# Performance work log

Hardware: AMD Instinct MI355X
Metric: run time of the kernel (lower is better)

Reference implementation:

```python
import jax, jax.numpy as jnp
import numpy as np

VOCAB = 50000
D = 256       # text_latent_size
E = 20000     # num_of_evidences
L = 20        # words_in_question / words per evidence sentence


def position_encoding(L, D):
    # encoding[i, j] = 1 - i/L - (j/D) * (1 - 2*i/L)
    i = jnp.arange(L, dtype=jnp.float32)[:, None] / L
    j = jnp.arange(D, dtype=jnp.float32)[None, :] / D
    return 1.0 - i - j * (1.0 - 2.0 * i)  # [L, D]


def setup_inputs() -> dict:
    key = jax.random.key(0)
    ks = jax.random.split(key, 8)
    evidence = jax.random.randint(ks[0], (E, L), 0, VOCAB)
    question = jax.random.randint(ks[1], (1, L), 0, VOCAB)
    scale = 0.05
    q_table = jax.random.normal(ks[2], (VOCAB, D), dtype=jnp.float32) * scale
    e_table = jax.random.normal(ks[3], (VOCAB, D), dtype=jnp.float32) * scale
    te1 = jax.random.normal(ks[4], (E, D), dtype=jnp.float32) * scale
    te2 = jax.random.normal(ks[5], (E, D), dtype=jnp.float32) * scale
    W = jax.random.normal(ks[6], (VOCAB, D), dtype=jnp.float32) * scale
    b = jax.random.normal(ks[7], (VOCAB,), dtype=jnp.float32) * scale
    return {"evidence": evidence, "question": question, "q_table": q_table,
            "e_table": e_table, "te1": te1, "te2": te2, "W": W, "b": b}


def reference(evidence, question, q_table, e_table, te1, te2, W, b):
    pe = position_encoding(L, D)                            # [L, D]
    # question: embed, position-encode, sum over words -> [D]
    q_emb = (q_table[question[0]] * pe).sum(axis=0)         # [D]
    # evidence: two embeddings, position-encode, sum over words -> [E, D]
    ev_comp = (q_table[evidence] * pe[None]).sum(axis=1) + te2  # [E, D]
    ev_feat = (e_table[evidence] * pe[None]).sum(axis=1) + te1  # [E, D]
    # attention over memories
    scores = ev_comp @ q_emb                                 # [E]
    weights = jax.nn.softmax(scores)                         # [E]
    weighted = weights @ ev_feat                             # [D]
    features = weighted + q_emb                              # [D]
    logits = features @ W.T + b                              # [VOCAB]
    return jax.nn.softmax(logits)
```

## Files before the change

### kernel.cpp

```cpp
#include <hip/hip_runtime.h>

#define D      256
#define L_W    20
#define E_CNT  20000
#define VOCAB  50000

#define CHUNK   1024
#define NCHUNK  49
#define NSLICE  8
#define RPS     (E_CNT / NSLICE)
#define PSTRIDE (NCHUNK * CHUNK)
#define WTB     256

#define OFF_QEMB  0
#define OFF_X     256
#define OFF_Y     512
#define OFF_WTE1  768
#define OFF_SUMW  1024
#define OFF_SUML  1025
#define OFF_A     1032
#define OFF_B     (OFF_A + VOCAB)
#define OFF_P     (OFF_B + VOCAB)
#define OFF_Q     (OFF_P + VOCAB)
#define OFF_EXPW  (OFF_Q + VOCAB)
#define OFF_EXPL  (OFF_EXPW + E_CNT)
#define OFF_PPART (OFF_EXPL + VOCAB)
#define OFF_QPART (OFF_PPART + NSLICE * PSTRIDE)
#define OFF_WTP   (OFF_QPART + NSLICE * PSTRIDE)
#define WS_FLOATS (OFF_WTP + WTB * D)

__device__ __forceinline__ float wave_reduce(float v) {
#pragma unroll
    for (int o = 32; o > 0; o >>= 1) v += __shfl_xor(v, o, 64);
    return v;
}

__device__ __forceinline__ float u_of(int j) { return 1.f - (float)j * (1.f / 128.f); }
__device__ __forceinline__ float s_of(int j) { return (float)j * (1.f / 256.f); }

__global__ void k1_qemb(const int* __restrict__ question,
                        const float* __restrict__ q_table,
                        float* __restrict__ ws) {
    __shared__ int sQ[L_W];
    int tid = threadIdx.x;
    if (tid < L_W) sQ[tid] = question[tid];
    __syncthreads();
    int j = tid;
    float u = u_of(j), s = s_of(j);
    float acc = 0.f;
#pragma unroll
    for (int i = 0; i < L_W; ++i) {
        float a = 1.f - (float)i * (1.f / (float)L_W);
        acc += q_table[(size_t)sQ[i] * D + j] * (a * u + s);
    }
    ws[OFF_QEMB + j] = acc;
    ws[OFF_X + j] = 0.f;
    ws[OFF_Y + j] = 0.f;
    ws[OFF_WTE1 + j] = 0.f;
    if (tid == 0) { ws[OFF_SUMW] = 0.f; ws[OFF_SUML] = 0.f; }
}

__global__ void k2_ab(const float* __restrict__ q_table, float* __restrict__ ws) {
    __shared__ float sQE[D];
    int tid = threadIdx.x;
    sQE[tid] = ws[OFF_QEMB + tid];
    __syncthreads();
    int wv = tid >> 6, lane = tid & 63;
    int v = blockIdx.x * 4 + wv;
    int j0 = lane * 4;
    const float4 q = *reinterpret_cast<const float4*>(&q_table[(size_t)v * D + j0]);
    float qe0 = sQE[j0], qe1 = sQE[j0 + 1], qe2 = sQE[j0 + 2], qe3 = sQE[j0 + 3];
    float accA = q.x * (u_of(j0) * qe0) + q.y * (u_of(j0 + 1) * qe1) +
                 q.z * (u_of(j0 + 2) * qe2) + q.w * (u_of(j0 + 3) * qe3);
    float accB = q.x * (s_of(j0) * qe0) + q.y * (s_of(j0 + 1) * qe1) +
                 q.z * (s_of(j0 + 2) * qe2) + q.w * (s_of(j0 + 3) * qe3);
    accA = wave_reduce(accA);
    accB = wave_reduce(accB);
    if (lane == 0) {
        ws[OFF_A + v] = accA;
        ws[OFF_B + v] = accB;
        ws[OFF_P + v] = 0.f;
        ws[OFF_Q + v] = 0.f;
    }
}

__global__ void k3_scores(const int* __restrict__ evidence,
                          const float* __restrict__ te2,
                          float* __restrict__ ws) {
    __shared__ float sQE[D];
    __shared__ float sPart[4];
    int tid = threadIdx.x;
    sQE[tid] = ws[OFF_QEMB + tid];
    __syncthreads();
    int wv = tid >> 6, lane = tid & 63;
    int gw = blockIdx.x * 4 + wv;
    int stride = gridDim.x * 4;
    int j0 = lane * 4;
    const float4 qe = *reinterpret_cast<const float4*>(&sQE[j0]);
    float wsum = 0.f;
    for (int e = gw; e < E_CNT; e += stride) {
        const float4 t = *reinterpret_cast<const float4*>(&te2[(size_t)e * D + j0]);
        float p = t.x * qe.x + t.y * qe.y + t.z * qe.z + t.w * qe.w;
        if (lane < 2 * L_W) {
            int l = (lane < L_W) ? lane : (lane - L_W);
            int idx = evidence[e * L_W + l];
            if (lane < L_W) {
                float a = 1.f - (float)l * (1.f / (float)L_W);
                p += a * ws[OFF_A + idx];
            } else {
                p += ws[OFF_B + idx];
            }
        }
        float s_e = wave_reduce(p);
        float ex = expf(s_e);
        if (lane == 0) ws[OFF_EXPW + e] = ex;
        wsum += ex;
    }
    if (lane == 0) sPart[wv] = wsum;
    __syncthreads();
    if (tid == 0) atomicAdd(&ws[OFF_SUMW], sPart[0] + sPart[1] + sPart[2] + sPart[3]);
}

__global__ void k5_scatter2(const int* __restrict__ evidence, float* __restrict__ ws) {
    __shared__ float sP[CHUNK], sQ[CHUNK];
    int tid = threadIdx.x;
    int chunk = blockIdx.x % NCHUNK;
    int slice = blockIdx.x / NCHUNK;
    for (int i = tid; i < CHUNK; i += 256) { sP[i] = 0.f; sQ[i] = 0.f; }
    __syncthreads();
    int lo = chunk * CHUNK;
    float inv = 1.f / ws[OFF_SUMW];
    int r0 = slice * RPS;
    for (int r = tid; r < RPS; r += 256) {
        int e = r0 + r;
        float w = ws[OFF_EXPW + e] * inv;
        const int4* rp = reinterpret_cast<const int4*>(evidence + (size_t)e * L_W);
        int4 v0 = rp[0], v1 = rp[1], v2 = rp[2], v3 = rp[3], v4 = rp[4];
        int idxs[L_W] = {v0.x, v0.y, v0.z, v0.w, v1.x, v1.y, v1.z, v1.w,
                         v2.x, v2.y, v2.z, v2.w, v3.x, v3.y, v3.z, v3.w,
                         v4.x, v4.y, v4.z, v4.w};
#pragma unroll
        for (int l = 0; l < L_W; ++l) {
            int d = idxs[l] - lo;
            if ((unsigned)d < (unsigned)CHUNK) {
                float a = 1.f - (float)l * (1.f / (float)L_W);
                atomicAdd(&sP[d], w * a);
                atomicAdd(&sQ[d], w);
            }
        }
    }
    __syncthreads();
    float* pp = &ws[OFF_PPART + (size_t)slice * PSTRIDE + (size_t)chunk * CHUNK];
    float* qp = &ws[OFF_QPART + (size_t)slice * PSTRIDE + (size_t)chunk * CHUNK];
    for (int i = tid; i < CHUNK; i += 256) { pp[i] = sP[i]; qp[i] = sQ[i]; }
}

__global__ void k5c_wte1(const float* __restrict__ te1, float* __restrict__ ws) {
    __shared__ float sWT[D];
    int tid = threadIdx.x;
    sWT[tid] = 0.f;
    __syncthreads();
    float inv = 1.f / ws[OFF_SUMW];
    int wv = tid >> 6, lane = tid & 63;
    int gw = blockIdx.x * 4 + wv;
    int stride = gridDim.x * 4;
    int j0 = lane * 4;
    float a0 = 0.f, a1 = 0.f, a2 = 0.f, a3 = 0.f;
    for (int e = gw; e < E_CNT; e += stride) {
        float w = ws[OFF_EXPW + e] * inv;
        const float4 t = *reinterpret_cast<const float4*>(&te1[(size_t)e * D + j0]);
        a0 += w * t.x; a1 += w * t.y; a2 += w * t.z; a3 += w * t.w;
    }
    atomicAdd(&sWT[j0 + 0], a0);
    atomicAdd(&sWT[j0 + 1], a1);
    atomicAdd(&sWT[j0 + 2], a2);
    atomicAdd(&sWT[j0 + 3], a3);
    __syncthreads();
    ws[OFF_WTP + blockIdx.x * D + tid] = sWT[tid];
}

__global__ void k5b_reduce(float* __restrict__ ws) {
    int tid = threadIdx.x;
    int v = blockIdx.x * 256 + tid;
    if (v < VOCAB) {
        float p = 0.f, q = 0.f;
#pragma unroll
        for (int s = 0; s < NSLICE; ++s) {
            p += ws[OFF_PPART + s * PSTRIDE + v];
            q += ws[OFF_QPART + s * PSTRIDE + v];
        }
        ws[OFF_P + v] = p;
        ws[OFF_Q + v] = q;
    }
    if (blockIdx.x == 0) {
        float acc = 0.f;
        for (int b = 0; b < WTB; ++b) acc += ws[OFF_WTP + b * D + tid];
        ws[OFF_WTE1 + tid] = acc;
    }
}

__global__ void k5_scatter(const int* __restrict__ evidence,
                           const float* __restrict__ te1,
                           float* __restrict__ ws) {
    __shared__ float sWT[D];
    int tid = threadIdx.x;
    sWT[tid] = 0.f;
    __syncthreads();
    float inv = 1.f / ws[OFF_SUMW];
    int wv = tid >> 6, lane = tid & 63;
    int gw = blockIdx.x * 4 + wv;
    int stride = gridDim.x * 4;
    int j0 = lane * 4;
    float a0 = 0.f, a1 = 0.f, a2 = 0.f, a3 = 0.f;
    for (int e = gw; e < E_CNT; e += stride) {
        float w = ws[OFF_EXPW + e] * inv;
        const float4 t = *reinterpret_cast<const float4*>(&te1[(size_t)e * D + j0]);
        a0 += w * t.x; a1 += w * t.y; a2 += w * t.z; a3 += w * t.w;
        if (lane < L_W) {
            int idx = evidence[e * L_W + lane];
            float a = 1.f - (float)lane * (1.f / (float)L_W);
            atomicAdd(&ws[OFF_P + idx], w * a);
            atomicAdd(&ws[OFF_Q + idx], w);
        }
    }
    atomicAdd(&sWT[j0 + 0], a0);
    atomicAdd(&sWT[j0 + 1], a1);
    atomicAdd(&sWT[j0 + 2], a2);
    atomicAdd(&sWT[j0 + 3], a3);
    __syncthreads();
    atomicAdd(&ws[OFF_WTE1 + tid], sWT[tid]);
}

__global__ void k6_xy(const float* __restrict__ e_table, float* __restrict__ ws) {
    __shared__ float sX[D], sY[D];
    int tid = threadIdx.x;
    sX[tid] = 0.f;
    sY[tid] = 0.f;
    __syncthreads();
    int wv = tid >> 6, lane = tid & 63;
    int gw = blockIdx.x * 4 + wv;
    int stride = gridDim.x * 4;
    int j0 = lane * 4;
    float x0 = 0.f, x1 = 0.f, x2 = 0.f, x3 = 0.f;
    float y0 = 0.f, y1 = 0.f, y2 = 0.f, y3 = 0.f;
    for (int v = gw; v < VOCAB; v += stride) {
        float P = ws[OFF_P + v];
        float Q = ws[OFF_Q + v];
        const float4 t = *reinterpret_cast<const float4*>(&e_table[(size_t)v * D + j0]);
        x0 += P * t.x; x1 += P * t.y; x2 += P * t.z; x3 += P * t.w;
        y0 += Q * t.x; y1 += Q * t.y; y2 += Q * t.z; y3 += Q * t.w;
    }
    atomicAdd(&sX[j0 + 0], x0); atomicAdd(&sX[j0 + 1], x1);
    atomicAdd(&sX[j0 + 2], x2); atomicAdd(&sX[j0 + 3], x3);
    atomicAdd(&sY[j0 + 0], y0); atomicAdd(&sY[j0 + 1], y1);
    atomicAdd(&sY[j0 + 2], y2); atomicAdd(&sY[j0 + 3], y3);
    __syncthreads();
    atomicAdd(&ws[OFF_X + tid], sX[tid]);
    atomicAdd(&ws[OFF_Y + tid], sY[tid]);
}

__global__ void k8_logits(const float* __restrict__ Wm, const float* __restrict__ bv,
                          float* __restrict__ ws) {
    __shared__ float sF[D];
    __shared__ float sPart[4];
    int tid = threadIdx.x;
    {
        int j = tid;
        sF[j] = u_of(j) * ws[OFF_X + j] + s_of(j) * ws[OFF_Y + j] +
                ws[OFF_WTE1 + j] + ws[OFF_QEMB + j];
    }
    __syncthreads();
    int wv = tid >> 6, lane = tid & 63;
    int gw = blockIdx.x * 4 + wv;
    int stride = gridDim.x * 4;
    int j0 = lane * 4;
    const float4 f = *reinterpret_cast<const float4*>(&sF[j0]);
    float lsum = 0.f;
    for (int v = gw; v < VOCAB; v += stride) {
        const float4 w4 = *reinterpret_cast<const float4*>(&Wm[(size_t)v * D + j0]);
        float p = w4.x * f.x + w4.y * f.y + w4.z * f.z + w4.w * f.w;
        float logit = wave_reduce(p) + bv[v];
        float ex = expf(logit);
        if (lane == 0) ws[OFF_EXPL + v] = ex;
        lsum += ex;
    }
    if (lane == 0) sPart[wv] = lsum;
    __syncthreads();
    if (tid == 0) atomicAdd(&ws[OFF_SUML], sPart[0] + sPart[1] + sPart[2] + sPart[3]);
}

__global__ void k10_norm(float* __restrict__ out, const float* __restrict__ ws) {
    int i = blockIdx.x * 256 + threadIdx.x;
    if (i < VOCAB) out[i] = ws[OFF_EXPL + i] * (1.f / ws[OFF_SUML]);
}

extern "C" void kernel_launch(void* const* d_in, const int* in_sizes, int n_in,
                              void* d_out, int out_size, void* d_ws, size_t ws_size,
                              hipStream_t stream) {
    const int*   evidence = (const int*)d_in[0];
    const int*   question = (const int*)d_in[1];
    const float* q_table  = (const float*)d_in[2];
    const float* e_table  = (const float*)d_in[3];
    const float* te1      = (const float*)d_in[4];
    const float* te2      = (const float*)d_in[5];
    const float* Wm       = (const float*)d_in[6];
    const float* bv       = (const float*)d_in[7];
    float* out = (float*)d_out;
    float* ws  = (float*)d_ws;

    const bool big = ws_size >= (size_t)WS_FLOATS * sizeof(float);

    k1_qemb<<<1, 256, 0, stream>>>(question, q_table, ws);
    k2_ab<<<VOCAB / 4, 256, 0, stream>>>(q_table, ws);
    k3_scores<<<512, 256, 0, stream>>>(evidence, te2, ws);
    if (big) {
        k5_scatter2<<<NCHUNK * NSLICE, 256, 0, stream>>>(evidence, ws);
        k5c_wte1<<<WTB, 256, 0, stream>>>(te1, ws);
        k5b_reduce<<<(VOCAB + 255) / 256, 256, 0, stream>>>(ws);
    } else {
        k5_scatter<<<512, 256, 0, stream>>>(evidence, te1, ws);
    }
    k6_xy<<<1024, 256, 0, stream>>>(e_table, ws);
    k8_logits<<<1024, 256, 0, stream>>>(Wm, bv, ws);
    k10_norm<<<(VOCAB + 255) / 256, 256, 0, stream>>>(out, ws);
}
```

Before: 296.0 us.

## Fuse te1 weighting into e_table pass and replace global atomics with partial reductions

The separate te1-weighted-sum kernel is removed and its work folded into the e_table X/Y accumulation kernel, which now walks a combined row range and processes four rows per iteration. Global float atomics for the softmax denominators and the X/Y accumulators become per-block partial buffers, reduced by a new reduction kernel or inside the consuming kernels. Softmax normalisation of the evidence weights is deferred to the logits kernel, and the scatter slice count is halved. This trades a kernel launch and atomic contention for an extra small reduction kernel and redundant per-block reductions in the logits and normalisation kernels.

```diff
diff --git a/kernel.cpp b/kernel.cpp
--- a/kernel.cpp
+++ b/kernel.cpp
@@ -4,21 +4,24 @@
 #define L_W    20
 #define E_CNT  20000
 #define VOCAB  50000
+#define TOTROW (VOCAB + E_CNT)
 
 #define CHUNK   1024
 #define NCHUNK  49
-#define NSLICE  8
+#define NSLICE  4
 #define RPS     (E_CNT / NSLICE)
 #define PSTRIDE (NCHUNK * CHUNK)
-#define WTB     256
+
+#define K6_BLOCKS 512
+#define K6_STRIDE 768
 
 #define OFF_QEMB  0
 #define OFF_X     256
 #define OFF_Y     512
 #define OFF_WTE1  768
-#define OFF_SUMW  1024
-#define OFF_SUML  1025
-#define OFF_A     1032
+#define OFF_SWP   1024
+#define OFF_LP    1536
+#define OFF_A     2560
 #define OFF_B     (OFF_A + VOCAB)
 #define OFF_P     (OFF_B + VOCAB)
 #define OFF_Q     (OFF_P + VOCAB)
@@ -26,8 +29,8 @@
 #define OFF_EXPL  (OFF_EXPW + E_CNT)
 #define OFF_PPART (OFF_EXPL + VOCAB)
 #define OFF_QPART (OFF_PPART + NSLICE * PSTRIDE)
-#define OFF_WTP   (OFF_QPART + NSLICE * PSTRIDE)
-#define WS_FLOATS (OFF_WTP + WTB * D)
+#define OFF_XYP   (OFF_QPART + NSLICE * PSTRIDE)
+#define WS_FLOATS (OFF_XYP + K6_BLOCKS * K6_STRIDE)
 
 __device__ __forceinline__ float wave_reduce(float v) {
 #pragma unroll
@@ -54,10 +57,6 @@
         acc += q_table[(size_t)sQ[i] * D + j] * (a * u + s);
     }
     ws[OFF_QEMB + j] = acc;
-    ws[OFF_X + j] = 0.f;
-    ws[OFF_Y + j] = 0.f;
-    ws[OFF_WTE1 + j] = 0.f;
-    if (tid == 0) { ws[OFF_SUMW] = 0.f; ws[OFF_SUML] = 0.f; }
 }
 
 __global__ void k2_ab(const float* __restrict__ q_table, float* __restrict__ ws) {
@@ -118,7 +117,7 @@
     }
     if (lane == 0) sPart[wv] = wsum;
     __syncthreads();
-    if (tid == 0) atomicAdd(&ws[OFF_SUMW], sPart[0] + sPart[1] + sPart[2] + sPart[3]);
+    if (tid == 0) ws[OFF_SWP + blockIdx.x] = sPart[0] + sPart[1] + sPart[2] + sPart[3];
 }
 
 __global__ void k5_scatter2(const int* __restrict__ evidence, float* __restrict__ ws) {
@@ -129,11 +128,10 @@
     for (int i = tid; i < CHUNK; i += 256) { sP[i] = 0.f; sQ[i] = 0.f; }
     __syncthreads();
     int lo = chunk * CHUNK;
-    float inv = 1.f / ws[OFF_SUMW];
     int r0 = slice * RPS;
     for (int r = tid; r < RPS; r += 256) {
         int e = r0 + r;
-        float w = ws[OFF_EXPW + e] * inv;
+        float w = ws[OFF_EXPW + e];
         const int4* rp = reinterpret_cast<const int4*>(evidence + (size_t)e * L_W);
         int4 v0 = rp[0], v1 = rp[1], v2 = rp[2], v3 = rp[3], v4 = rp[4];
         int idxs[L_W] = {v0.x, v0.y, v0.z, v0.w, v1.x, v1.y, v1.z, v1.w,
@@ -155,33 +153,8 @@
     for (int i = tid; i < CHUNK; i += 256) { pp[i] = sP[i]; qp[i] = sQ[i]; }
 }
 
-__global__ void k5c_wte1(const float* __restrict__ te1, float* __restrict__ ws) {
-    __shared__ float sWT[D];
-    int tid = threadIdx.x;
-    sWT[tid] = 0.f;
-    __syncthreads();
-    float inv = 1.f / ws[OFF_SUMW];
-    int wv = tid >> 6, lane = tid & 63;
-    int gw = blockIdx.x * 4 + wv;
-    int stride = gridDim.x * 4;
-    int j0 = lane * 4;
-    float a0 = 0.f, a1 = 0.f, a2 = 0.f, a3 = 0.f;
-    for (int e = gw; e < E_CNT; e += stride) {
-        float w = ws[OFF_EXPW + e] * inv;
-        const float4 t = *reinterpret_cast<const float4*>(&te1[(size_t)e * D + j0]);
-        a0 += w * t.x; a1 += w * t.y; a2 += w * t.z; a3 += w * t.w;
-    }
-    atomicAdd(&sWT[j0 + 0], a0);
-    atomicAdd(&sWT[j0 + 1], a1);
-    atomicAdd(&sWT[j0 + 2], a2);
-    atomicAdd(&sWT[j0 + 3], a3);
-    __syncthreads();
-    ws[OFF_WTP + blockIdx.x * D + tid] = sWT[tid];
-}
-
 __global__ void k5b_reduce(float* __restrict__ ws) {
-    int tid = threadIdx.x;
-    int v = blockIdx.x * 256 + tid;
+    int v = blockIdx.x * 256 + threadIdx.x;
     if (v < VOCAB) {
         float p = 0.f, q = 0.f;
 #pragma unroll
@@ -192,30 +165,15 @@
         ws[OFF_P + v] = p;
         ws[OFF_Q + v] = q;
     }
-    if (blockIdx.x == 0) {
-        float acc = 0.f;
-        for (int b = 0; b < WTB; ++b) acc += ws[OFF_WTP + b * D + tid];
-        ws[OFF_WTE1 + tid] = acc;
-    }
-}
-
-__global__ void k5_scatter(const int* __restrict__ evidence,
-                           const float* __restrict__ te1,
-                           float* __restrict__ ws) {
-    __shared__ float sWT[D];
-    int tid = threadIdx.x;
-    sWT[tid] = 0.f;
-    __syncthreads();
-    float inv = 1.f / ws[OFF_SUMW];
+}
+
+__global__ void k5_scatter(const int* __restrict__ evidence, float* __restrict__ ws) {
+    int tid = threadIdx.x;
     int wv = tid >> 6, lane = tid & 63;
     int gw = blockIdx.x * 4 + wv;
     int stride = gridDim.x * 4;
-    int j0 = lane * 4;
-    float a0 = 0.f, a1 = 0.f, a2 = 0.f, a3 = 0.f;
     for (int e = gw; e < E_CNT; e += stride) {
-        float w = ws[OFF_EXPW + e] * inv;
-        const float4 t = *reinterpret_cast<const float4*>(&te1[(size_t)e * D + j0]);
-        a0 += w * t.x; a1 += w * t.y; a2 += w * t.z; a3 += w * t.w;
+        float w = ws[OFF_EXPW + e];
         if (lane < L_W) {
             int idx = evidence[e * L_W + lane];
             float a = 1.f - (float)lane * (1.f / (float)L_W);
@@ -223,52 +181,109 @@
             atomicAdd(&ws[OFF_Q + idx], w);
         }
     }
-    atomicAdd(&sWT[j0 + 0], a0);
-    atomicAdd(&sWT[j0 + 1], a1);
-    atomicAdd(&sWT[j0 + 2], a2);
-    atomicAdd(&sWT[j0 + 3], a3);
-    __syncthreads();
-    atomicAdd(&ws[OFF_WTE1 + tid], sWT[tid]);
-}
-
-__global__ void k6_xy(const float* __restrict__ e_table, float* __restrict__ ws) {
-    __shared__ float sX[D], sY[D];
-    int tid = threadIdx.x;
-    sX[tid] = 0.f;
-    sY[tid] = 0.f;
+}
+
+__global__ void k6_xyt(const float* __restrict__ e_table,
+                       const float* __restrict__ te1,
+                       float* __restrict__ ws) {
+    __shared__ float sAcc[K6_STRIDE];
+    int tid = threadIdx.x;
+    for (int i = tid; i < K6_STRIDE; i += 256) sAcc[i] = 0.f;
     __syncthreads();
     int wv = tid >> 6, lane = tid & 63;
     int gw = blockIdx.x * 4 + wv;
-    int stride = gridDim.x * 4;
+    int nw = gridDim.x * 4;
     int j0 = lane * 4;
     float x0 = 0.f, x1 = 0.f, x2 = 0.f, x3 = 0.f;
     float y0 = 0.f, y1 = 0.f, y2 = 0.f, y3 = 0.f;
-    for (int v = gw; v < VOCAB; v += stride) {
-        float P = ws[OFF_P + v];
-        float Q = ws[OFF_Q + v];
-        const float4 t = *reinterpret_cast<const float4*>(&e_table[(size_t)v * D + j0]);
-        x0 += P * t.x; x1 += P * t.y; x2 += P * t.z; x3 += P * t.w;
-        y0 += Q * t.x; y1 += Q * t.y; y2 += Q * t.z; y3 += Q * t.w;
-    }
-    atomicAdd(&sX[j0 + 0], x0); atomicAdd(&sX[j0 + 1], x1);
-    atomicAdd(&sX[j0 + 2], x2); atomicAdd(&sX[j0 + 3], x3);
-    atomicAdd(&sY[j0 + 0], y0); atomicAdd(&sY[j0 + 1], y1);
-    atomicAdd(&sY[j0 + 2], y2); atomicAdd(&sY[j0 + 3], y3);
-    __syncthreads();
-    atomicAdd(&ws[OFF_X + tid], sX[tid]);
-    atomicAdd(&ws[OFF_Y + tid], sY[tid]);
+    float t0 = 0.f, t1 = 0.f, t2 = 0.f, t3 = 0.f;
+    for (int v0 = gw * 4; v0 < TOTROW; v0 += nw * 4) {
+        if (v0 < VOCAB) {
+            const float4 P4 = *reinterpret_cast<const float4*>(&ws[OFF_P + v0]);
+            const float4 Q4 = *reinterpret_cast<const float4*>(&ws[OFF_Q + v0]);
+            const float4 r0 = *reinterpret_cast<const float4*>(&e_table[(size_t)(v0 + 0) * D + j0]);
+            const float4 r1 = *reinterpret_cast<const float4*>(&e_table[(size_t)(v0 + 1) * D + j0]);
+            const float4 r2 = *reinterpret_cast<const float4*>(&e_table[(size_t)(v0 + 2) * D + j0]);
+            const float4 r3 = *reinterpret_cast<const float4*>(&e_table[(size_t)(v0 + 3) * D + j0]);
+            x0 += P4.x * r0.x + P4.y * r1.x + P4.z * r2.x + P4.w * r3.x;
+            x1 += P4.x * r0.y + P4.y * r1.y + P4.z * r2.y + P4.w * r3.y;
+            x2 += P4.x * r0.z + P4.y * r1.z + P4.z * r2.z + P4.w * r3.z;
+            x3 += P4.x * r0.w + P4.y * r1.w + P4.z * r2.w + P4.w * r3.w;
+            y0 += Q4.x * r0.x + Q4.y * r1.x + Q4.z * r2.x + Q4.w * r3.x;
+            y1 += Q4.x * r0.y + Q4.y * r1.y + Q4.z * r2.y + Q4.w * r3.y;
+            y2 += Q4.x * r0.z + Q4.y * r1.z + Q4.z * r2.z + Q4.w * r3.z;
+            y3 += Q4.x * r0.w + Q4.y * r1.w + Q4.z * r2.w + Q4.w * r3.w;
+        } else {
+            int e0 = v0 - VOCAB;
+            const float4 W4 = *reinterpret_cast<const float4*>(&ws[OFF_EXPW + e0]);
+            const float4 r0 = *reinterpret_cast<const float4*>(&te1[(size_t)(e0 + 0) * D + j0]);
+            const float4 r1 = *reinterpret_cast<const float4*>(&te1[(size_t)(e0 + 1) * D + j0]);
+            const float4 r2 = *reinterpret_cast<const float4*>(&te1[(size_t)(e0 + 2) * D + j0]);
+            const float4 r3 = *reinterpret_cast<const float4*>(&te1[(size_t)(e0 + 3) * D + j0]);
+            t0 += W4.x * r0.x + W4.y * r1.x + W4.z * r2.x + W4.w * r3.x;
+            t1 += W4.x * r0.y + W4.y * r1.y + W4.z * r2.y + W4.w * r3.y;
+            t2 += W4.x * r0.z + W4.y * r1.z + W4.z * r2.z + W4.w * r3.z;
+            t3 += W4.x * r0.w + W4.y * r1.w + W4.z * r2.w + W4.w * r3.w;
+        }
+    }
+    atomicAdd(&sAcc[j0 + 0], x0); atomicAdd(&sAcc[j0 + 1], x1);
+    atomicAdd(&sAcc[j0 + 2], x2); atomicAdd(&sAcc[j0 + 3], x3);
+    atomicAdd(&sAcc[256 + j0 + 0], y0); atomicAdd(&sAcc[256 + j0 + 1], y1);
+    atomicAdd(&sAcc[256 + j0 + 2], y2); atomicAdd(&sAcc[256 + j0 + 3], y3);
+    atomicAdd(&sAcc[512 + j0 + 0], t0); atomicAdd(&sAcc[512 + j0 + 1], t1);
+    atomicAdd(&sAcc[512 + j0 + 2], t2); atomicAdd(&sAcc[512 + j0 + 3], t3);
+    __syncthreads();
+    float* base = &ws[OFF_XYP + (size_t)blockIdx.x * K6_STRIDE];
+    for (int i = tid; i < K6_STRIDE; i += 256) base[i] = sAcc[i];
+}
+
+__global__ void k6b_reduce(float* __restrict__ ws) {
+    __shared__ float sR[256 * 4];
+    int tid = threadIdx.x;
+    int s0 = blockIdx.x * 4;
+    float a0 = 0.f, a1 = 0.f, a2 = 0.f, a3 = 0.f;
+#pragma unroll
+    for (int r = 0; r < K6_BLOCKS / 256; ++r) {
+        int b = tid + r * 256;
+        const float4 v = *reinterpret_cast<const float4*>(&ws[OFF_XYP + (size_t)b * K6_STRIDE + s0]);
+        a0 += v.x; a1 += v.y; a2 += v.z; a3 += v.w;
+    }
+    sR[tid * 4 + 0] = a0; sR[tid * 4 + 1] = a1;
+    sR[tid * 4 + 2] = a2; sR[tid * 4 + 3] = a3;
+    __syncthreads();
+#pragma unroll
+    for (int off = 128; off > 0; off >>= 1) {
+        if (tid < off) {
+#pragma unroll
+            for (int c = 0; c < 4; ++c) sR[tid * 4 + c] += sR[(tid + off) * 4 + c];
+        }
+        __syncthreads();
+    }
+    if (tid < 4) {
+        int s = s0 + tid;
+        float v = sR[tid];
+        if (s < 256)      ws[OFF_X + s] = v;
+        else if (s < 512) ws[OFF_Y + s - 256] = v;
+        else              ws[OFF_WTE1 + s - 512] = v;
+    }
 }
 
 __global__ void k8_logits(const float* __restrict__ Wm, const float* __restrict__ bv,
                           float* __restrict__ ws) {
     __shared__ float sF[D];
+    __shared__ float sRed[256];
     __shared__ float sPart[4];
     int tid = threadIdx.x;
-    {
-        int j = tid;
-        sF[j] = u_of(j) * ws[OFF_X + j] + s_of(j) * ws[OFF_Y + j] +
-                ws[OFF_WTE1 + j] + ws[OFF_QEMB + j];
-    }
+    sRed[tid] = ws[OFF_SWP + tid] + ws[OFF_SWP + 256 + tid];
+    __syncthreads();
+#pragma unroll
+    for (int off = 128; off > 0; off >>= 1) {
+        if (tid < off) sRed[tid] += sRed[tid + off];
+        __syncthreads();
+    }
+    float invw = 1.f / sRed[0];
+    sF[tid] = (u_of(tid) * ws[OFF_X + tid] + s_of(tid) * ws[OFF_Y + tid] +
+               ws[OFF_WTE1 + tid]) * invw + ws[OFF_QEMB + tid];
     __syncthreads();
     int wv = tid >> 6, lane = tid & 63;
     int gw = blockIdx.x * 4 + wv;
@@ -286,12 +301,25 @@
     }
     if (lane == 0) sPart[wv] = lsum;
     __syncthreads();
-    if (tid == 0) atomicAdd(&ws[OFF_SUML], sPart[0] + sPart[1] + sPart[2] + sPart[3]);
+    if (tid == 0) ws[OFF_LP + blockIdx.x] = sPart[0] + sPart[1] + sPart[2] + sPart[3];
 }
 
 __global__ void k10_norm(float* __restrict__ out, const float* __restrict__ ws) {
-    int i = blockIdx.x * 256 + threadIdx.x;
-    if (i < VOCAB) out[i] = ws[OFF_EXPL + i] * (1.f / ws[OFF_SUML]);
+    __shared__ float sRed[256];
+    int tid = threadIdx.x;
+    float l = 0.f;
+#pragma unroll
+    for (int r = 0; r < 4; ++r) l += ws[OFF_LP + tid + r * 256];
+    sRed[tid] = l;
+    __syncthreads();
+#pragma unroll
+    for (int off = 128; off > 0; off >>= 1) {
+        if (tid < off) sRed[tid] += sRed[tid + off];
+        __syncthreads();
+    }
+    float invL = 1.f / sRed[0];
+    int i = blockIdx.x * 256 + tid;
+    if (i < VOCAB) out[i] = ws[OFF_EXPL + i] * invL;
 }
 
 extern "C" void kernel_launch(void* const* d_in, const int* in_sizes, int n_in,
@@ -315,12 +343,12 @@
     k3_scores<<<512, 256, 0, stream>>>(evidence, te2, ws);
     if (big) {
         k5_scatter2<<<NCHUNK * NSLICE, 256, 0, stream>>>(evidence, ws);
-        k5c_wte1<<<WTB, 256, 0, stream>>>(te1, ws);
         k5b_reduce<<<(VOCAB + 255) / 256, 256, 0, stream>>>(ws);
     } else {
-        k5_scatter<<<512, 256, 0, stream>>>(evidence, te1, ws);
-    }
-    k6_xy<<<1024, 256, 0, stream>>>(e_table, ws);
+        k5_scatter<<<512, 256, 0, stream>>>(evidence, ws);
+    }
+    k6_xyt<<<K6_BLOCKS, 256, 0, stream>>>(e_table, te1, ws);
+    k6b_reduce<<<K6_STRIDE / 4, 256, 0, stream>>>(ws);
     k8_logits<<<1024, 256, 0, stream>>>(Wm, bv, ws);
     k10_norm<<<(VOCAB + 255) / 256, 256, 0, stream>>>(out, ws);
 }
```

After: 256.6 us. -13.3%, faster.
